# Kernel optimization log

Hardware: AMD Instinct MI355X
Metric: run time of the kernel (lower is better)

## Reference

```python
import jax, jax.numpy as jnp
import numpy as np

# HistogramQuantizer(percentile=99.99, gamma=0.99, n_bits=8, eps=0.0, act_decay=0.01), training mode
PERCENTILE = 99.99 / 100.0
GAMMA = 0.99
Q_MAX = float(2 ** (8 - 1) - 1)  # 127.0
EPS = 0.0
CLAMP_INIT = 100.0  # registered buffer initial value


def setup_inputs() -> dict:
    key = jax.random.key(0)
    x = jax.random.normal(key, (4, 4096, 4096), dtype=jnp.float32)
    return {"x": x}


def reference(x):
    x_abs = jnp.abs(x)
    # --- training-path percentile via full sort (quantile_from_sorted) ---
    flat = jnp.sort(x_abs.ravel())
    n = flat.size  # static
    k = int(round(PERCENTILE * n)) - 1
    clamp_value = flat[k]
    # EMA buffer update (side state; returned so the sort is not dead code)
    new_buffer = CLAMP_INIT * GAMMA + clamp_value * (1.0 - GAMMA)
    # --- fake quantization (Quantizer.forward with q_max=Q_MAX) ---
    # note: x_max/clamp_value only affects the backward mask, not the forward math
    scale = Q_MAX / jnp.maximum(jnp.max(x_abs), EPS)
    out = jnp.clip(jnp.round(x * scale), -Q_MAX, Q_MAX) / scale
    return out, new_buffer
```

## Files before the change

### kernel.cpp

```cpp
#include <hip/hip_runtime.h>
#include <math.h>

#define WS_MAXBITS 0
#define WS_SELBIN  1
#define WS_RANK    2
#define WS_HIST    4
#define HIST_WORDS 4096
#define WS_BMAX    4100
#define WS_CNT     5124
#define WS_CAND    6160
#define NBLK       1024
#define CAP        256

typedef float floatx4 __attribute__((ext_vector_type(4)));

extern "C" __global__ void __launch_bounds__(256)
k_max_hist(const float* __restrict__ x, long n, unsigned int* __restrict__ ws) {
    __shared__ unsigned int lhist[HIST_WORDS];
    __shared__ unsigned int wred[4];
    for (int i = threadIdx.x; i < HIST_WORDS; i += 256) lhist[i] = 0;
    __syncthreads();

    long n4 = n >> 2;
    const float4* x4 = (const float4*)x;
    unsigned int mymax = 0;
    long stride = (long)gridDim.x * 256;
    long i = (long)blockIdx.x * 256 + threadIdx.x;
    for (; i + stride < n4; i += 2 * stride) {
        float4 v0 = x4[i];
        float4 v1 = x4[i + stride];
        unsigned int a0 = __float_as_uint(fabsf(v0.x));
        unsigned int a1 = __float_as_uint(fabsf(v0.y));
        unsigned int a2 = __float_as_uint(fabsf(v0.z));
        unsigned int a3 = __float_as_uint(fabsf(v0.w));
        unsigned int b0 = __float_as_uint(fabsf(v1.x));
        unsigned int b1 = __float_as_uint(fabsf(v1.y));
        unsigned int b2 = __float_as_uint(fabsf(v1.z));
        unsigned int b3 = __float_as_uint(fabsf(v1.w));
        mymax = max(mymax, max(max(a0, a1), max(a2, a3)));
        mymax = max(mymax, max(max(b0, b1), max(b2, b3)));
        atomicAdd(&lhist[a0 >> 20], 1u);
        atomicAdd(&lhist[a1 >> 20], 1u);
        atomicAdd(&lhist[a2 >> 20], 1u);
        atomicAdd(&lhist[a3 >> 20], 1u);
        atomicAdd(&lhist[b0 >> 20], 1u);
        atomicAdd(&lhist[b1 >> 20], 1u);
        atomicAdd(&lhist[b2 >> 20], 1u);
        atomicAdd(&lhist[b3 >> 20], 1u);
    }
    for (; i < n4; i += stride) {
        float4 v = x4[i];
        unsigned int a0 = __float_as_uint(fabsf(v.x));
        unsigned int a1 = __float_as_uint(fabsf(v.y));
        unsigned int a2 = __float_as_uint(fabsf(v.z));
        unsigned int a3 = __float_as_uint(fabsf(v.w));
        mymax = max(mymax, max(max(a0, a1), max(a2, a3)));
        atomicAdd(&lhist[a0 >> 20], 1u);
        atomicAdd(&lhist[a1 >> 20], 1u);
        atomicAdd(&lhist[a2 >> 20], 1u);
        atomicAdd(&lhist[a3 >> 20], 1u);
    }
    if (blockIdx.x == 0 && threadIdx.x < (int)(n & 3)) {
        unsigned int a = __float_as_uint(fabsf(x[n4 * 4 + threadIdx.x]));
        mymax = max(mymax, a);
        atomicAdd(&lhist[a >> 20], 1u);
    }

    for (int off = 32; off > 0; off >>= 1)
        mymax = max(mymax, __shfl_down(mymax, off, 64));
    int lane = threadIdx.x & 63, wid = threadIdx.x >> 6;
    if (lane == 0) wred[wid] = mymax;
    __syncthreads();
    if (threadIdx.x == 0) {
        ws[WS_BMAX + blockIdx.x] =
            max(max(wred[0], wred[1]), max(wred[2], wred[3]));
    }
    unsigned int rot = (blockIdx.x * 1297u) & (HIST_WORDS - 1);
    for (int idx = threadIdx.x; idx < HIST_WORDS; idx += 256) {
        unsigned int bin = (idx + rot) & (HIST_WORDS - 1);
        unsigned int c = lhist[bin];
        if (c) atomicAdd(&ws[WS_HIST + bin], c);
    }
}

extern "C" __global__ void __launch_bounds__(256)
k_scan(unsigned int* __restrict__ ws, long k) {
    __shared__ unsigned long long partial[256];
    __shared__ unsigned int mred[256];
    const unsigned int* hist = ws + WS_HIST;

    unsigned int m = 0;
    for (int s = threadIdx.x; s < NBLK; s += 256) m = max(m, ws[WS_BMAX + s]);
    mred[threadIdx.x] = m;

    int base = threadIdx.x * (HIST_WORDS / 256);
    unsigned long long s = 0;
    for (int i = 0; i < 16; i++) s += hist[base + i];
    partial[threadIdx.x] = s;
    __syncthreads();
    if (threadIdx.x == 0) {
        unsigned int mm = 0;
        for (int t = 0; t < 256; t++) mm = max(mm, mred[t]);
        ws[WS_MAXBITS] = mm;

        unsigned long long acc = 0;
        long bin = -1;
        unsigned long long before = 0;
        for (int t = 0; t < 256; t++) {
            unsigned long long ps = partial[t];
            if (bin < 0 && acc + ps > (unsigned long long)k) {
                unsigned long long a2 = acc;
                for (int i = 0; i < 16; i++) {
                    unsigned int c = hist[t * 16 + i];
                    if (a2 + c > (unsigned long long)k) { bin = t * 16 + i; before = a2; break; }
                    a2 += c;
                }
            }
            acc += ps;
        }
        ws[WS_SELBIN] = (unsigned int)bin;
        ws[WS_RANK]   = (unsigned int)((unsigned long long)k - before);
    }
}

extern "C" __global__ void __launch_bounds__(256)
k_quant(const float* __restrict__ x, float* __restrict__ out, long n,
        unsigned int* __restrict__ ws) {
    __shared__ unsigned int lbuf[CAP];
    __shared__ unsigned int lcnt;
    if (threadIdx.x == 0) lcnt = 0;
    __syncthreads();

    float xmax = __uint_as_float(ws[WS_MAXBITS]);
    unsigned int selbin = ws[WS_SELBIN];
    float scale = 127.0f / xmax;
    float inv = 1.0f / scale;

    long n4 = n >> 2;
    const float4* x4 = (const float4*)x;
    floatx4* out4 = (floatx4*)out;
    long stride = (long)gridDim.x * 256;
    long i = (long)blockIdx.x * 256 + threadIdx.x;
    for (; i + stride < n4; i += 2 * stride) {
        float4 v0 = x4[i];
        float4 v1 = x4[i + stride];
        floatx4 r0, r1;
        r0.x = fminf(fmaxf(rintf(v0.x * scale), -127.0f), 127.0f) * inv;
        r0.y = fminf(fmaxf(rintf(v0.y * scale), -127.0f), 127.0f) * inv;
        r0.z = fminf(fmaxf(rintf(v0.z * scale), -127.0f), 127.0f) * inv;
        r0.w = fminf(fmaxf(rintf(v0.w * scale), -127.0f), 127.0f) * inv;
        r1.x = fminf(fmaxf(rintf(v1.x * scale), -127.0f), 127.0f) * inv;
        r1.y = fminf(fmaxf(rintf(v1.y * scale), -127.0f), 127.0f) * inv;
        r1.z = fminf(fmaxf(rintf(v1.z * scale), -127.0f), 127.0f) * inv;
        r1.w = fminf(fmaxf(rintf(v1.w * scale), -127.0f), 127.0f) * inv;
        __builtin_nontemporal_store(r0, &out4[i]);
        __builtin_nontemporal_store(r1, &out4[i + stride]);
        unsigned int a0 = __float_as_uint(fabsf(v0.x));
        unsigned int a1 = __float_as_uint(fabsf(v0.y));
        unsigned int a2 = __float_as_uint(fabsf(v0.z));
        unsigned int a3 = __float_as_uint(fabsf(v0.w));
        unsigned int b0 = __float_as_uint(fabsf(v1.x));
        unsigned int b1 = __float_as_uint(fabsf(v1.y));
        unsigned int b2 = __float_as_uint(fabsf(v1.z));
        unsigned int b3 = __float_as_uint(fabsf(v1.w));
        if ((a0 >> 20) == selbin) { unsigned int p = atomicAdd(&lcnt, 1u); if (p < CAP) lbuf[p] = a0; }
        if ((a1 >> 20) == selbin) { unsigned int p = atomicAdd(&lcnt, 1u); if (p < CAP) lbuf[p] = a1; }
        if ((a2 >> 20) == selbin) { unsigned int p = atomicAdd(&lcnt, 1u); if (p < CAP) lbuf[p] = a2; }
        if ((a3 >> 20) == selbin) { unsigned int p = atomicAdd(&lcnt, 1u); if (p < CAP) lbuf[p] = a3; }
        if ((b0 >> 20) == selbin) { unsigned int p = atomicAdd(&lcnt, 1u); if (p < CAP) lbuf[p] = b0; }
        if ((b1 >> 20) == selbin) { unsigned int p = atomicAdd(&lcnt, 1u); if (p < CAP) lbuf[p] = b1; }
        if ((b2 >> 20) == selbin) { unsigned int p = atomicAdd(&lcnt, 1u); if (p < CAP) lbuf[p] = b2; }
        if ((b3 >> 20) == selbin) { unsigned int p = atomicAdd(&lcnt, 1u); if (p < CAP) lbuf[p] = b3; }
    }
    for (; i < n4; i += stride) {
        float4 v = x4[i];
        floatx4 r;
        r.x = fminf(fmaxf(rintf(v.x * scale), -127.0f), 127.0f) * inv;
        r.y = fminf(fmaxf(rintf(v.y * scale), -127.0f), 127.0f) * inv;
        r.z = fminf(fmaxf(rintf(v.z * scale), -127.0f), 127.0f) * inv;
        r.w = fminf(fmaxf(rintf(v.w * scale), -127.0f), 127.0f) * inv;
        __builtin_nontemporal_store(r, &out4[i]);
        unsigned int a0 = __float_as_uint(fabsf(v.x));
        unsigned int a1 = __float_as_uint(fabsf(v.y));
        unsigned int a2 = __float_as_uint(fabsf(v.z));
        unsigned int a3 = __float_as_uint(fabsf(v.w));
        if ((a0 >> 20) == selbin) { unsigned int p = atomicAdd(&lcnt, 1u); if (p < CAP) lbuf[p] = a0; }
        if ((a1 >> 20) == selbin) { unsigned int p = atomicAdd(&lcnt, 1u); if (p < CAP) lbuf[p] = a1; }
        if ((a2 >> 20) == selbin) { unsigned int p = atomicAdd(&lcnt, 1u); if (p < CAP) lbuf[p] = a2; }
        if ((a3 >> 20) == selbin) { unsigned int p = atomicAdd(&lcnt, 1u); if (p < CAP) lbuf[p] = a3; }
    }
    if (blockIdx.x == 0 && threadIdx.x < (int)(n & 3)) {
        long t = n4 * 4 + threadIdx.x;
        float v = x[t];
        out[t] = fminf(fmaxf(rintf(v * scale), -127.0f), 127.0f) * inv;
        unsigned int a = __float_as_uint(fabsf(v));
        if ((a >> 20) == selbin) { unsigned int p = atomicAdd(&lcnt, 1u); if (p < CAP) lbuf[p] = a; }
    }
    __syncthreads();
    unsigned int c = lcnt; if (c > CAP) c = CAP;
    unsigned int* seg = ws + WS_CAND + (unsigned int)blockIdx.x * CAP;
    for (unsigned int e = threadIdx.x; e < c; e += 256) seg[e] = lbuf[e];
    if (threadIdx.x == 0) ws[WS_CNT + blockIdx.x] = c;
}

extern "C" __global__ void __launch_bounds__(256)
k_select(unsigned int* __restrict__ ws, float* __restrict__ out_last) {
    __shared__ unsigned int hist[1024];
    __shared__ unsigned int s_b1, s_j2;
    unsigned int j = ws[WS_RANK];
    unsigned int selbin = ws[WS_SELBIN];

    for (int i = threadIdx.x; i < 1024; i += 256) hist[i] = 0;
    __syncthreads();
    for (int s = threadIdx.x; s < NBLK; s += 256) {
        unsigned int c = ws[WS_CNT + s]; if (c > CAP) c = CAP;
        const unsigned int* seg = ws + WS_CAND + (unsigned int)s * CAP;
        for (unsigned int e = 0; e < c; e++)
            atomicAdd(&hist[(seg[e] >> 10) & 1023], 1u);
    }
    __syncthreads();
    if (threadIdx.x == 0) {
        unsigned int acc = 0, b1 = 1023;
        for (int b = 0; b < 1024; b++) {
            unsigned int h = hist[b];
            if (acc + h > j) { b1 = (unsigned int)b; break; }
            acc += h;
        }
        s_b1 = b1; s_j2 = j - acc;
    }
    __syncthreads();
    unsigned int pref = (selbin << 10) | s_b1;
    unsigned int j2 = s_j2;
    for (int i = threadIdx.x; i < 1024; i += 256) hist[i] = 0;
    __syncthreads();
    for (int s = threadIdx.x; s < NBLK; s += 256) {
        unsigned int c = ws[WS_CNT + s]; if (c > CAP) c = CAP;
        const unsigned int* seg = ws + WS_CAND + (unsigned int)s * CAP;
        for (unsigned int e = 0; e < c; e++) {
            unsigned int u = seg[e];
            if ((u >> 10) == pref) atomicAdd(&hist[u & 1023], 1u);
        }
    }
    __syncthreads();
    if (threadIdx.x == 0) {
        unsigned int acc = 0, b2 = 1023;
        for (int b = 0; b < 1024; b++) {
            unsigned int h = hist[b];
            if (acc + h > j2) { b2 = (unsigned int)b; break; }
            acc += h;
        }
        float clampv = __uint_as_float((pref << 10) | b2);
        out_last[0] = (float)(100.0 * 0.99 + (double)clampv * 0.01);
    }
}

extern "C" void kernel_launch(void* const* d_in, const int* in_sizes, int n_in,
                              void* d_out, int out_size, void* d_ws, size_t ws_size,
                              hipStream_t stream) {
    const float* x = (const float*)d_in[0];
    long n = (long)in_sizes[0];
    float* out = (float*)d_out;
    unsigned int* ws = (unsigned int*)d_ws;

    long k = (long)llround((99.99 / 100.0) * (double)n) - 1;
    if (k < 0) k = 0;
    if (k >= n) k = n - 1;

    (void)hipMemsetAsync((char*)d_ws + WS_HIST * sizeof(unsigned int), 0,
                         HIST_WORDS * sizeof(unsigned int), stream);

    k_max_hist<<<NBLK, 256, 0, stream>>>(x, n, ws);
    k_scan<<<1, 256, 0, stream>>>(ws, k);
    k_quant<<<NBLK, 256, 0, stream>>>(x, out, n, ws);
    k_select<<<1, 256, 0, stream>>>(ws, out + n);
}
```

Before: 588.5 us.

## Fuse scan and select into last-block tails, double grid, unroll loads by four

The single-block scan and select kernels are folded into the tails of the two streaming passes. Each block increments an agent-scope atomic done counter, and the last block to finish does the reduction and selection, which removes two kernel launches and their gaps. The grid doubles to 2048 blocks and each thread loads four float4 per iteration instead of two, to get more memory-level parallelism. The cost is extra shared memory per block (the extra state adds about 3 KB in pass1 and 4 KB in pass2) and a serial tail run by one block; the memset now also clears the done counters.

```diff
diff --git a/kernel.cpp b/kernel.cpp
--- a/kernel.cpp
+++ b/kernel.cpp
@@ -4,20 +4,29 @@
 #define WS_MAXBITS 0
 #define WS_SELBIN  1
 #define WS_RANK    2
-#define WS_HIST    4
+#define WS_DONE1   3
+#define WS_DONE2   4
+#define WS_HIST    8
 #define HIST_WORDS 4096
-#define WS_BMAX    4100
-#define WS_CNT     5124
-#define WS_CAND    6160
-#define NBLK       1024
+#define WS_BMAX    (WS_HIST + HIST_WORDS)
+#define WS_CNT     (WS_BMAX + NBLK)
+#define WS_CAND    (WS_CNT + NBLK)
+#define NBLK       2048
 #define CAP        256
 
 typedef float floatx4 __attribute__((ext_vector_type(4)));
 
+__device__ __forceinline__ unsigned int agent_inc_acqrel(unsigned int* p) {
+    return __hip_atomic_fetch_add(p, 1u, __ATOMIC_ACQ_REL, __HIP_MEMORY_SCOPE_AGENT);
+}
+
 extern "C" __global__ void __launch_bounds__(256)
-k_max_hist(const float* __restrict__ x, long n, unsigned int* __restrict__ ws) {
+k_pass1(const float* __restrict__ x, long n, unsigned int* __restrict__ ws, long k) {
     __shared__ unsigned int lhist[HIST_WORDS];
     __shared__ unsigned int wred[4];
+    __shared__ unsigned int s_last;
+    __shared__ unsigned long long partial[256];
+    __shared__ unsigned int mred[256];
     for (int i = threadIdx.x; i < HIST_WORDS; i += 256) lhist[i] = 0;
     __syncthreads();
 
@@ -26,34 +35,40 @@
     unsigned int mymax = 0;
     long stride = (long)gridDim.x * 256;
     long i = (long)blockIdx.x * 256 + threadIdx.x;
-    for (; i + stride < n4; i += 2 * stride) {
+    for (; i + 3 * stride < n4; i += 4 * stride) {
         float4 v0 = x4[i];
         float4 v1 = x4[i + stride];
-        unsigned int a0 = __float_as_uint(fabsf(v0.x));
-        unsigned int a1 = __float_as_uint(fabsf(v0.y));
-        unsigned int a2 = __float_as_uint(fabsf(v0.z));
-        unsigned int a3 = __float_as_uint(fabsf(v0.w));
-        unsigned int b0 = __float_as_uint(fabsf(v1.x));
-        unsigned int b1 = __float_as_uint(fabsf(v1.y));
-        unsigned int b2 = __float_as_uint(fabsf(v1.z));
-        unsigned int b3 = __float_as_uint(fabsf(v1.w));
-        mymax = max(mymax, max(max(a0, a1), max(a2, a3)));
-        mymax = max(mymax, max(max(b0, b1), max(b2, b3)));
-        atomicAdd(&lhist[a0 >> 20], 1u);
-        atomicAdd(&lhist[a1 >> 20], 1u);
-        atomicAdd(&lhist[a2 >> 20], 1u);
-        atomicAdd(&lhist[a3 >> 20], 1u);
-        atomicAdd(&lhist[b0 >> 20], 1u);
-        atomicAdd(&lhist[b1 >> 20], 1u);
-        atomicAdd(&lhist[b2 >> 20], 1u);
-        atomicAdd(&lhist[b3 >> 20], 1u);
+        float4 v2 = x4[i + 2 * stride];
+        float4 v3 = x4[i + 3 * stride];
+        unsigned int a[16];
+        a[0]  = __float_as_uint(v0.x) & 0x7fffffffu;
+        a[1]  = __float_as_uint(v0.y) & 0x7fffffffu;
+        a[2]  = __float_as_uint(v0.z) & 0x7fffffffu;
+        a[3]  = __float_as_uint(v0.w) & 0x7fffffffu;
+        a[4]  = __float_as_uint(v1.x) & 0x7fffffffu;
+        a[5]  = __float_as_uint(v1.y) & 0x7fffffffu;
+        a[6]  = __float_as_uint(v1.z) & 0x7fffffffu;
+        a[7]  = __float_as_uint(v1.w) & 0x7fffffffu;
+        a[8]  = __float_as_uint(v2.x) & 0x7fffffffu;
+        a[9]  = __float_as_uint(v2.y) & 0x7fffffffu;
+        a[10] = __float_as_uint(v2.z) & 0x7fffffffu;
+        a[11] = __float_as_uint(v2.w) & 0x7fffffffu;
+        a[12] = __float_as_uint(v3.x) & 0x7fffffffu;
+        a[13] = __float_as_uint(v3.y) & 0x7fffffffu;
+        a[14] = __float_as_uint(v3.z) & 0x7fffffffu;
+        a[15] = __float_as_uint(v3.w) & 0x7fffffffu;
+        #pragma unroll
+        for (int e = 0; e < 16; e++) {
+            mymax = max(mymax, a[e]);
+            atomicAdd(&lhist[a[e] >> 20], 1u);
+        }
     }
     for (; i < n4; i += stride) {
         float4 v = x4[i];
-        unsigned int a0 = __float_as_uint(fabsf(v.x));
-        unsigned int a1 = __float_as_uint(fabsf(v.y));
-        unsigned int a2 = __float_as_uint(fabsf(v.z));
-        unsigned int a3 = __float_as_uint(fabsf(v.w));
+        unsigned int a0 = __float_as_uint(v.x) & 0x7fffffffu;
+        unsigned int a1 = __float_as_uint(v.y) & 0x7fffffffu;
+        unsigned int a2 = __float_as_uint(v.z) & 0x7fffffffu;
+        unsigned int a3 = __float_as_uint(v.w) & 0x7fffffffu;
         mymax = max(mymax, max(max(a0, a1), max(a2, a3)));
         atomicAdd(&lhist[a0 >> 20], 1u);
         atomicAdd(&lhist[a1 >> 20], 1u);
@@ -61,7 +76,7 @@
         atomicAdd(&lhist[a3 >> 20], 1u);
     }
     if (blockIdx.x == 0 && threadIdx.x < (int)(n & 3)) {
-        unsigned int a = __float_as_uint(fabsf(x[n4 * 4 + threadIdx.x]));
+        unsigned int a = __float_as_uint(x[n4 * 4 + threadIdx.x]) & 0x7fffffffu;
         mymax = max(mymax, a);
         atomicAdd(&lhist[a >> 20], 1u);
     }
@@ -81,38 +96,35 @@
         unsigned int c = lhist[bin];
         if (c) atomicAdd(&ws[WS_HIST + bin], c);
     }
-}
-
-extern "C" __global__ void __launch_bounds__(256)
-k_scan(unsigned int* __restrict__ ws, long k) {
-    __shared__ unsigned long long partial[256];
-    __shared__ unsigned int mred[256];
+
+    __threadfence();
+    __syncthreads();
+    if (threadIdx.x == 0)
+        s_last = (agent_inc_acqrel(&ws[WS_DONE1]) == (unsigned int)(gridDim.x - 1));
+    __syncthreads();
+    if (!s_last) return;
+    unsigned int m = 0;
+    for (int s2 = threadIdx.x; s2 < NBLK; s2 += 256) m = max(m, ws[WS_BMAX + s2]);
+    mred[threadIdx.x] = m;
     const unsigned int* hist = ws + WS_HIST;
-
-    unsigned int m = 0;
-    for (int s = threadIdx.x; s < NBLK; s += 256) m = max(m, ws[WS_BMAX + s]);
-    mred[threadIdx.x] = m;
-
     int base = threadIdx.x * (HIST_WORDS / 256);
     unsigned long long s = 0;
-    for (int i = 0; i < 16; i++) s += hist[base + i];
+    for (int t = 0; t < 16; t++) s += hist[base + t];
     partial[threadIdx.x] = s;
     __syncthreads();
     if (threadIdx.x == 0) {
         unsigned int mm = 0;
         for (int t = 0; t < 256; t++) mm = max(mm, mred[t]);
         ws[WS_MAXBITS] = mm;
-
-        unsigned long long acc = 0;
+        unsigned long long acc = 0, before = 0;
         long bin = -1;
-        unsigned long long before = 0;
         for (int t = 0; t < 256; t++) {
             unsigned long long ps = partial[t];
             if (bin < 0 && acc + ps > (unsigned long long)k) {
                 unsigned long long a2 = acc;
-                for (int i = 0; i < 16; i++) {
-                    unsigned int c = hist[t * 16 + i];
-                    if (a2 + c > (unsigned long long)k) { bin = t * 16 + i; before = a2; break; }
+                for (int q = 0; q < 16; q++) {
+                    unsigned int c = hist[t * 16 + q];
+                    if (a2 + c > (unsigned long long)k) { bin = t * 16 + q; before = a2; break; }
                     a2 += c;
                 }
             }
@@ -124,10 +136,13 @@
 }
 
 extern "C" __global__ void __launch_bounds__(256)
-k_quant(const float* __restrict__ x, float* __restrict__ out, long n,
+k_pass2(const float* __restrict__ x, float* __restrict__ out, long n,
         unsigned int* __restrict__ ws) {
     __shared__ unsigned int lbuf[CAP];
     __shared__ unsigned int lcnt;
+    __shared__ unsigned int s_last;
+    __shared__ unsigned int hist[1024];
+    __shared__ unsigned int s_b1, s_j2;
     if (threadIdx.x == 0) lcnt = 0;
     __syncthreads();
 
@@ -141,10 +156,12 @@
     floatx4* out4 = (floatx4*)out;
     long stride = (long)gridDim.x * 256;
     long i = (long)blockIdx.x * 256 + threadIdx.x;
-    for (; i + stride < n4; i += 2 * stride) {
+    for (; i + 3 * stride < n4; i += 4 * stride) {
         float4 v0 = x4[i];
         float4 v1 = x4[i + stride];
-        floatx4 r0, r1;
+        float4 v2 = x4[i + 2 * stride];
+        float4 v3 = x4[i + 3 * stride];
+        floatx4 r0, r1, r2, r3;
         r0.x = fminf(fmaxf(rintf(v0.x * scale), -127.0f), 127.0f) * inv;
         r0.y = fminf(fmaxf(rintf(v0.y * scale), -127.0f), 127.0f) * inv;
         r0.z = fminf(fmaxf(rintf(v0.z * scale), -127.0f), 127.0f) * inv;
@@ -153,24 +170,42 @@
         r1.y = fminf(fmaxf(rintf(v1.y * scale), -127.0f), 127.0f) * inv;
         r1.z = fminf(fmaxf(rintf(v1.z * scale), -127.0f), 127.0f) * inv;
         r1.w = fminf(fmaxf(rintf(v1.w * scale), -127.0f), 127.0f) * inv;
+        r2.x = fminf(fmaxf(rintf(v2.x * scale), -127.0f), 127.0f) * inv;
+        r2.y = fminf(fmaxf(rintf(v2.y * scale), -127.0f), 127.0f) * inv;
+        r2.z = fminf(fmaxf(rintf(v2.z * scale), -127.0f), 127.0f) * inv;
+        r2.w = fminf(fmaxf(rintf(v2.w * scale), -127.0f), 127.0f) * inv;
+        r3.x = fminf(fmaxf(rintf(v3.x * scale), -127.0f), 127.0f) * inv;
+        r3.y = fminf(fmaxf(rintf(v3.y * scale), -127.0f), 127.0f) * inv;
+        r3.z = fminf(fmaxf(rintf(v3.z * scale), -127.0f), 127.0f) * inv;
+        r3.w = fminf(fmaxf(rintf(v3.w * scale), -127.0f), 127.0f) * inv;
         __builtin_nontemporal_store(r0, &out4[i]);
         __builtin_nontemporal_store(r1, &out4[i + stride]);
-        unsigned int a0 = __float_as_uint(fabsf(v0.x));
-        unsigned int a1 = __float_as_uint(fabsf(v0.y));
-        unsigned int a2 = __float_as_uint(fabsf(v0.z));
-        unsigned int a3 = __float_as_uint(fabsf(v0.w));
-        unsigned int b0 = __float_as_uint(fabsf(v1.x));
-        unsigned int b1 = __float_as_uint(fabsf(v1.y));
-        unsigned int b2 = __float_as_uint(fabsf(v1.z));
-        unsigned int b3 = __float_as_uint(fabsf(v1.w));
-        if ((a0 >> 20) == selbin) { unsigned int p = atomicAdd(&lcnt, 1u); if (p < CAP) lbuf[p] = a0; }
-        if ((a1 >> 20) == selbin) { unsigned int p = atomicAdd(&lcnt, 1u); if (p < CAP) lbuf[p] = a1; }
-        if ((a2 >> 20) == selbin) { unsigned int p = atomicAdd(&lcnt, 1u); if (p < CAP) lbuf[p] = a2; }
-        if ((a3 >> 20) == selbin) { unsigned int p = atomicAdd(&lcnt, 1u); if (p < CAP) lbuf[p] = a3; }
-        if ((b0 >> 20) == selbin) { unsigned int p = atomicAdd(&lcnt, 1u); if (p < CAP) lbuf[p] = b0; }
-        if ((b1 >> 20) == selbin) { unsigned int p = atomicAdd(&lcnt, 1u); if (p < CAP) lbuf[p] = b1; }
-        if ((b2 >> 20) == selbin) { unsigned int p = atomicAdd(&lcnt, 1u); if (p < CAP) lbuf[p] = b2; }
-        if ((b3 >> 20) == selbin) { unsigned int p = atomicAdd(&lcnt, 1u); if (p < CAP) lbuf[p] = b3; }
+        __builtin_nontemporal_store(r2, &out4[i + 2 * stride]);
+        __builtin_nontemporal_store(r3, &out4[i + 3 * stride]);
+        unsigned int a[16];
+        a[0]  = __float_as_uint(v0.x) & 0x7fffffffu;
+        a[1]  = __float_as_uint(v0.y) & 0x7fffffffu;
+        a[2]  = __float_as_uint(v0.z) & 0x7fffffffu;
+        a[3]  = __float_as_uint(v0.w) & 0x7fffffffu;
+        a[4]  = __float_as_uint(v1.x) & 0x7fffffffu;
+        a[5]  = __float_as_uint(v1.y) & 0x7fffffffu;
+        a[6]  = __float_as_uint(v1.z) & 0x7fffffffu;
+        a[7]  = __float_as_uint(v1.w) & 0x7fffffffu;
+        a[8]  = __float_as_uint(v2.x) & 0x7fffffffu;
+        a[9]  = __float_as_uint(v2.y) & 0x7fffffffu;
+        a[10] = __float_as_uint(v2.z) & 0x7fffffffu;
+        a[11] = __float_as_uint(v2.w) & 0x7fffffffu;
+        a[12] = __float_as_uint(v3.x) & 0x7fffffffu;
+        a[13] = __float_as_uint(v3.y) & 0x7fffffffu;
+        a[14] = __float_as_uint(v3.z) & 0x7fffffffu;
+        a[15] = __float_as_uint(v3.w) & 0x7fffffffu;
+        #pragma unroll
+        for (int e = 0; e < 16; e++) {
+            if ((a[e] >> 20) == selbin) {
+                unsigned int p = atomicAdd(&lcnt, 1u);
+                if (p < CAP) lbuf[p] = a[e];
+            }
+        }
     }
     for (; i < n4; i += stride) {
         float4 v = x4[i];
@@ -180,10 +215,10 @@
         r.z = fminf(fmaxf(rintf(v.z * scale), -127.0f), 127.0f) * inv;
         r.w = fminf(fmaxf(rintf(v.w * scale), -127.0f), 127.0f) * inv;
         __builtin_nontemporal_store(r, &out4[i]);
-        unsigned int a0 = __float_as_uint(fabsf(v.x));
-        unsigned int a1 = __float_as_uint(fabsf(v.y));
-        unsigned int a2 = __float_as_uint(fabsf(v.z));
-        unsigned int a3 = __float_as_uint(fabsf(v.w));
+        unsigned int a0 = __float_as_uint(v.x) & 0x7fffffffu;
+        unsigned int a1 = __float_as_uint(v.y) & 0x7fffffffu;
+        unsigned int a2 = __float_as_uint(v.z) & 0x7fffffffu;
+        unsigned int a3 = __float_as_uint(v.w) & 0x7fffffffu;
         if ((a0 >> 20) == selbin) { unsigned int p = atomicAdd(&lcnt, 1u); if (p < CAP) lbuf[p] = a0; }
         if ((a1 >> 20) == selbin) { unsigned int p = atomicAdd(&lcnt, 1u); if (p < CAP) lbuf[p] = a1; }
         if ((a2 >> 20) == selbin) { unsigned int p = atomicAdd(&lcnt, 1u); if (p < CAP) lbuf[p] = a2; }
@@ -193,7 +228,7 @@
         long t = n4 * 4 + threadIdx.x;
         float v = x[t];
         out[t] = fminf(fmaxf(rintf(v * scale), -127.0f), 127.0f) * inv;
-        unsigned int a = __float_as_uint(fabsf(v));
+        unsigned int a = __float_as_uint(v) & 0x7fffffffu;
         if ((a >> 20) == selbin) { unsigned int p = atomicAdd(&lcnt, 1u); if (p < CAP) lbuf[p] = a; }
     }
     __syncthreads();
@@ -201,22 +236,22 @@
     unsigned int* seg = ws + WS_CAND + (unsigned int)blockIdx.x * CAP;
     for (unsigned int e = threadIdx.x; e < c; e += 256) seg[e] = lbuf[e];
     if (threadIdx.x == 0) ws[WS_CNT + blockIdx.x] = c;
-}
-
-extern "C" __global__ void __launch_bounds__(256)
-k_select(unsigned int* __restrict__ ws, float* __restrict__ out_last) {
-    __shared__ unsigned int hist[1024];
-    __shared__ unsigned int s_b1, s_j2;
+
+    __threadfence();
+    __syncthreads();
+    if (threadIdx.x == 0)
+        s_last = (agent_inc_acqrel(&ws[WS_DONE2]) == (unsigned int)(gridDim.x - 1));
+    __syncthreads();
+    if (!s_last) return;
+
     unsigned int j = ws[WS_RANK];
-    unsigned int selbin = ws[WS_SELBIN];
-
-    for (int i = threadIdx.x; i < 1024; i += 256) hist[i] = 0;
-    __syncthreads();
-    for (int s = threadIdx.x; s < NBLK; s += 256) {
-        unsigned int c = ws[WS_CNT + s]; if (c > CAP) c = CAP;
-        const unsigned int* seg = ws + WS_CAND + (unsigned int)s * CAP;
-        for (unsigned int e = 0; e < c; e++)
-            atomicAdd(&hist[(seg[e] >> 10) & 1023], 1u);
+    for (int q = threadIdx.x; q < 1024; q += 256) hist[q] = 0;
+    __syncthreads();
+    for (int s2 = threadIdx.x; s2 < NBLK; s2 += 256) {
+        unsigned int cc = ws[WS_CNT + s2]; if (cc > CAP) cc = CAP;
+        const unsigned int* sg = ws + WS_CAND + (unsigned int)s2 * CAP;
+        for (unsigned int e = 0; e < cc; e++)
+            atomicAdd(&hist[(sg[e] >> 10) & 1023], 1u);
     }
     __syncthreads();
     if (threadIdx.x == 0) {
@@ -231,13 +266,13 @@
     __syncthreads();
     unsigned int pref = (selbin << 10) | s_b1;
     unsigned int j2 = s_j2;
-    for (int i = threadIdx.x; i < 1024; i += 256) hist[i] = 0;
-    __syncthreads();
-    for (int s = threadIdx.x; s < NBLK; s += 256) {
-        unsigned int c = ws[WS_CNT + s]; if (c > CAP) c = CAP;
-        const unsigned int* seg = ws + WS_CAND + (unsigned int)s * CAP;
-        for (unsigned int e = 0; e < c; e++) {
-            unsigned int u = seg[e];
+    for (int q = threadIdx.x; q < 1024; q += 256) hist[q] = 0;
+    __syncthreads();
+    for (int s2 = threadIdx.x; s2 < NBLK; s2 += 256) {
+        unsigned int cc = ws[WS_CNT + s2]; if (cc > CAP) cc = CAP;
+        const unsigned int* sg = ws + WS_CAND + (unsigned int)s2 * CAP;
+        for (unsigned int e = 0; e < cc; e++) {
+            unsigned int u = sg[e];
             if ((u >> 10) == pref) atomicAdd(&hist[u & 1023], 1u);
         }
     }
@@ -250,7 +285,7 @@
             acc += h;
         }
         float clampv = __uint_as_float((pref << 10) | b2);
-        out_last[0] = (float)(100.0 * 0.99 + (double)clampv * 0.01);
+        out[n] = (float)(100.0 * 0.99 + (double)clampv * 0.01);
     }
 }
 
@@ -266,11 +301,8 @@
     if (k < 0) k = 0;
     if (k >= n) k = n - 1;
 
-    (void)hipMemsetAsync((char*)d_ws + WS_HIST * sizeof(unsigned int), 0,
-                         HIST_WORDS * sizeof(unsigned int), stream);
-
-    k_max_hist<<<NBLK, 256, 0, stream>>>(x, n, ws);
-    k_scan<<<1, 256, 0, stream>>>(ws, k);
-    k_quant<<<NBLK, 256, 0, stream>>>(x, out, n, ws);
-    k_select<<<1, 256, 0, stream>>>(ws, out + n);
+    (void)hipMemsetAsync(d_ws, 0, (WS_HIST + HIST_WORDS) * sizeof(unsigned int), stream);
+
+    k_pass1<<<NBLK, 256, 0, stream>>>(x, n, ws, k);
+    k_pass2<<<NBLK, 256, 0, stream>>>(x, out, n, ws);
 }
```

Measured after the change: 1.152 ms. +95.8%, slower.
